# Kernel optimization log

Hardware: AMD Instinct MI355X
Metric: run time of the kernel (lower is better)

The kernel has to match this reference:

```python
import jax, jax.numpy as jnp
import numpy as np

N, D_IN, D_OUT = 8192, 1024, 1024

def setup_inputs() -> dict:
    key = jax.random.key(0)
    k1, k2, k3, k4 = jax.random.split(key, 4)
    scale = 1.0 / np.sqrt(D_IN).astype(np.float32)
    return {
        "X": jax.random.normal(k1, (N, D_IN), dtype=jnp.float32),
        "W_Q": jax.random.normal(k2, (D_IN, D_OUT), dtype=jnp.float32) * scale,
        "W_K": jax.random.normal(k3, (D_IN, D_OUT), dtype=jnp.float32) * scale,
        "W_V": jax.random.normal(k4, (D_IN, D_OUT), dtype=jnp.float32) * scale,
    }

def reference(X, W_Q, W_K, W_V):
    # Manual single-head self-attention over the N rows of X.
    Q = X @ W_Q            # [N, d_out]
    Kmat = X @ W_K         # [N, d_out]
    V = X @ W_V            # [N, d_out]
    inv_sqrt_d = jnp.asarray(1.0 / np.sqrt(W_Q.shape[1]), dtype=Q.dtype)
    scores = (Q @ Kmat.T) * inv_sqrt_d            # [N, N]
    attn = jax.nn.softmax(scores, axis=-1)        # row-wise softmax (Keras default axis=-1)
    return attn @ V                               # [N, d_out]
```

## Files before the change

kernel.cpp:

```cpp
#include <hip/hip_runtime.h>

#define N_ROWS 8192
#define D_DIM  1024
#define SM_SHIFT 4.0f

typedef _Float16 f16;
typedef _Float16 f16x8 __attribute__((ext_vector_type(8)));
typedef _Float16 f16x4 __attribute__((ext_vector_type(4)));
typedef float    f32x4 __attribute__((ext_vector_type(4)));

__device__ __forceinline__ void gload16(const void* g, void* l) {
  __builtin_amdgcn_global_load_lds(
      (const __attribute__((address_space(1))) void*)g,
      (__attribute__((address_space(3))) void*)l, 16, 0, 0);
}

__device__ __forceinline__ int xcd_swz(int bid, int nb) {
  return (bid & 7) * (nb >> 3) + (bid >> 3);
}

__device__ __forceinline__ void tile2d4(int bid, int ny_t, int& nx, int& ny) {
  const int v = xcd_swz(bid, 32 * ny_t);
  const int g = v >> 4, w = v & 15;
  const int gpc = ny_t >> 2;
  const int gx = g / gpc, gy = g - gx * gpc;
  nx = gx * 4 + (w & 3);
  ny = gy * 4 + (w >> 2);
}

__global__ __launch_bounds__(256) void f32_to_f16_kernel(
    const float* __restrict__ in, f16* __restrict__ out, int n4) {
  for (int i = blockIdx.x * blockDim.x + threadIdx.x; i < n4;
       i += gridDim.x * blockDim.x) {
    float4 x = ((const float4*)in)[i];
    f16x4 h = {(f16)x.x, (f16)x.y, (f16)x.z, (f16)x.w};
    ((f16x4*)out)[i] = h;
  }
}

__global__ __launch_bounds__(256) void transpose_w_kernel(
    const float* __restrict__ w0, const float* __restrict__ w1,
    const float* __restrict__ w2, f16* __restrict__ WT) {
  const float* W = (blockIdx.z == 0) ? w0 : (blockIdx.z == 1) ? w1 : w2;
  f16* T = WT + (size_t)blockIdx.z * D_DIM * D_DIM;
  __shared__ float tile[64][65];
  const int r0 = blockIdx.y * 64, c0 = blockIdx.x * 64;
  const int t = threadIdx.x;
#pragma unroll
  for (int rep = 0; rep < 16; ++rep) {
    int idx = rep * 256 + t;
    int r = idx >> 6, c = idx & 63;
    tile[r][c] = W[(size_t)(r0 + r) * D_DIM + (c0 + c)];
  }
  __syncthreads();
#pragma unroll
  for (int rep = 0; rep < 16; ++rep) {
    int idx = rep * 256 + t;
    int r = idx >> 6, c = idx & 63;
    T[(size_t)(c0 + r) * D_DIM + (r0 + c)] = (f16)tile[c][r];
  }
}

template <bool SWAP>
__device__ __forceinline__ void mainloop256(const f16* __restrict__ Ag, int lda,
                                            const f16* __restrict__ Bg,
                                            int ldbt, int nk, f16* LA, f16* LB,
                                            f32x4 (&acc)[8][4], int tid) {
  const int lane = tid & 63;
  const int wr = tid >> 8, wc = (tid >> 6) & 3;
  const int ro = lane & 15;
  const int jj0 = (((lane >> 4) ^ (ro & 7)) << 4);
  const int rs = tid >> 3;
  const int ce = ((tid & 7) ^ (rs & 7)) * 8;
  const f16* a[4];
  const f16* b[4];
#pragma unroll
  for (int s = 0; s < 4; ++s) {
    a[s] = Ag + (size_t)(rs + 64 * s) * lda + ce;
    b[s] = Bg + (size_t)(rs + 64 * s) * ldbt + ce;
  }
  char* la = (char*)LA;
  char* lb = (char*)LB;
  const int t16 = tid * 16;

  auto stage = [&](int buf) {
    char* A = la + buf * 32768;
    char* B = lb + buf * 32768;
#pragma unroll
    for (int s = 0; s < 4; ++s) {
      gload16(a[s], A + s * 8192 + t16);
      gload16(b[s], B + s * 8192 + t16);
    }
#pragma unroll
    for (int s = 0; s < 4; ++s) {
      a[s] += 64;
      b[s] += 64;
    }
  };

  f16x8 af[4], bf[4];
  auto readA = [&](const char* ab, int h, int jo) {
#pragma unroll
    for (int j = 0; j < 4; ++j)
      af[j] = *(const f16x8*)(ab + (wr * 128 + h * 64 + j * 16 + ro) * 128 + jo);
  };
  auto readB = [&](const char* bb, int jo) {
#pragma unroll
    for (int ni = 0; ni < 4; ++ni)
      bf[ni] = *(const f16x8*)(bb + (wc * 64 + ni * 16 + ro) * 128 + jo);
  };

#define PHASE_TAIL(H)                                                     \
  __builtin_amdgcn_s_barrier();                                           \
  __builtin_amdgcn_sched_barrier(0);                                      \
  asm volatile("s_waitcnt lgkmcnt(0)" ::: "memory");                      \
  __builtin_amdgcn_sched_barrier(0);                                      \
  __builtin_amdgcn_s_setprio(1);                                          \
  _Pragma("unroll") for (int j = 0; j < 4; ++j)                           \
  _Pragma("unroll") for (int ni = 0; ni < 4; ++ni)                        \
      acc[(H) * 4 + j][ni] =                                              \
          SWAP ? __builtin_amdgcn_mfma_f32_16x16x32_f16(bf[ni], af[j],    \
                                                        acc[(H) * 4 + j][ni], \
                                                        0, 0, 0)          \
               : __builtin_amdgcn_mfma_f32_16x16x32_f16(af[j], bf[ni],    \
                                                        acc[(H) * 4 + j][ni], \
                                                        0, 0, 0);         \
  __builtin_amdgcn_s_setprio(0);

  stage(0);
  if (nk > 1) {
    stage(1);
    asm volatile("s_waitcnt vmcnt(8)" ::: "memory");
  } else {
    asm volatile("s_waitcnt vmcnt(0)" ::: "memory");
  }
  __builtin_amdgcn_s_barrier();
  __builtin_amdgcn_sched_barrier(0);

  for (int kt = 0; kt < nk; ++kt) {
    const int buf = kt & 1;
    const char* ab = la + buf * 32768;
    const char* bb = lb + buf * 32768;
    readA(ab, 0, jj0);
    readB(bb, jj0);
    PHASE_TAIL(0)
    readA(ab, 1, jj0);
    PHASE_TAIL(1)
    readA(ab, 0, jj0 ^ 64);
    readB(bb, jj0 ^ 64);
    PHASE_TAIL(0)
    readA(ab, 1, jj0 ^ 64);
    PHASE_TAIL(1)
    __builtin_amdgcn_s_barrier();
    __builtin_amdgcn_sched_barrier(0);
    if (kt + 2 < nk) stage(buf);
    if (kt + 1 < nk) {
      if (kt + 2 < nk)
        asm volatile("s_waitcnt vmcnt(8)" ::: "memory");
      else
        asm volatile("s_waitcnt vmcnt(0)" ::: "memory");
      __builtin_amdgcn_s_barrier();
      __builtin_amdgcn_sched_barrier(0);
    }
  }
#undef PHASE_TAIL
}

#define ACC_INIT8(acc)                                \
  _Pragma("unroll") for (int i = 0; i < 8; ++i)       \
      _Pragma("unroll") for (int j = 0; j < 4; ++j)   \
          acc[i][j] = (f32x4){0.f, 0.f, 0.f, 0.f};

__global__ __launch_bounds__(512, 2) void gemm_qkv(
    const f16* __restrict__ Xh, const f16* __restrict__ WT,
    f16* __restrict__ Q, f16* __restrict__ Kh, f16* __restrict__ VT) {
  __shared__ f16 LA[2][16384], LB[2][16384];
  const int v = xcd_swz(blockIdx.x, 384);
  const int z = v >> 7, r = v & 127;
  const int nx = r & 3, ny = r >> 2;
  const int tid = threadIdx.x, lane = tid & 63;
  const int wr = tid >> 8, wc = (tid >> 6) & 3;
  const int ro = lane & 15, rq = (lane >> 4) * 4;

  const f16* A = Xh + (size_t)ny * 256 * D_DIM;
  const f16* B = WT + (size_t)z * D_DIM * D_DIM + (size_t)nx * 256 * D_DIM;

  f32x4 acc[8][4];
  ACC_INIT8(acc);
  if (z < 2) {
    mainloop256<true>(A, D_DIM, B, D_DIM, D_DIM / 64, &LA[0][0], &LB[0][0],
                      acc, tid);
    f16* C = z ? Kh : Q;
#pragma unroll
    for (int mi = 0; mi < 8; ++mi) {
      const size_t xr = ny * 256 + wr * 128 + mi * 16 + ro;
#pragma unroll
      for (int ni = 0; ni < 4; ++ni) {
        f16x4 pk;
#pragma unroll
        for (int rr = 0; rr < 4; ++rr) pk[rr] = (f16)acc[mi][ni][rr];
        *(f16x4*)&C[xr * D_DIM + nx * 256 + wc * 64 + ni * 16 + rq] = pk;
      }
    }
  } else {
    mainloop256<false>(A, D_DIM, B, D_DIM, D_DIM / 64, &LA[0][0], &LB[0][0],
                       acc, tid);
#pragma unroll
    for (int mi = 0; mi < 8; ++mi)
#pragma unroll
      for (int ni = 0; ni < 4; ++ni) {
        f16x4 pk;
#pragma unroll
        for (int rr = 0; rr < 4; ++rr) pk[rr] = (f16)acc[mi][ni][rr];
        const size_t d = nx * 256 + wc * 64 + ni * 16 + ro;
        *(f16x4*)&VT[d * N_ROWS + ny * 256 + wr * 128 + mi * 16 + rq] = pk;
      }
  }
}

__global__ __launch_bounds__(512, 2) void gemm_s_exp(
    const f16* __restrict__ Q, const f16* __restrict__ Kh, f16* __restrict__ S,
    float* __restrict__ Lpart, int nyb) {
  __shared__ f16 LA[2][16384], LB[2][16384];
  int nx, ny;
  tile2d4(blockIdx.x, nyb, nx, ny);
  const int tid = threadIdx.x, lane = tid & 63;
  const int wr = tid >> 8, wc = (tid >> 6) & 3;
  const int ro = lane & 15, rq = (lane >> 4) * 4;

  f32x4 acc[8][4];
  ACC_INIT8(acc);
  mainloop256<true>(Q + (size_t)ny * 256 * D_DIM, D_DIM,
                    Kh + (size_t)nx * 256 * D_DIM, D_DIM, D_DIM / 64,
                    &LA[0][0], &LB[0][0], acc, tid);

  const float sc = 0.03125f;
#pragma unroll
  for (int mi = 0; mi < 8; ++mi) {
    const size_t q = ny * 256 + wr * 128 + mi * 16 + ro;
    f16* srow = S + q * N_ROWS + nx * 256 + wc * 64 + rq;
    float rs = 0.f;
#pragma unroll
    for (int ni = 0; ni < 4; ++ni) {
      f16x4 pk;
#pragma unroll
      for (int rr = 0; rr < 4; ++rr) {
        const float p = __expf(acc[mi][ni][rr] * sc - SM_SHIFT);
        rs += p;
        pk[rr] = (f16)p;
      }
      *(f16x4*)&srow[ni * 16] = pk;
    }
    rs += __shfl_xor(rs, 16, 64);
    rs += __shfl_xor(rs, 32, 64);
    if (lane < 16) Lpart[q * 128 + nx * 4 + wc] = rs;
  }
}

__global__ __launch_bounds__(256) void reduce_l(const float* __restrict__ Lpart,
                                                float* __restrict__ linv,
                                                int rows) {
  const int w = (blockIdx.x * 256 + threadIdx.x) >> 6;
  const int lane = threadIdx.x & 63;
  if (w >= rows) return;
  const float* p = Lpart + (size_t)w * 128;
  float s = p[lane] + p[lane + 64];
#pragma unroll
  for (int o = 32; o > 0; o >>= 1) s += __shfl_xor(s, o, 64);
  if (lane == 0) linv[w] = 1.0f / s;
}

__global__ __launch_bounds__(512, 2) void gemm_pv(const f16* __restrict__ S,
                                                  const f16* __restrict__ VT,
                                                  float* __restrict__ Ppart,
                                                  int nyb, int KS, int chunk) {
  __shared__ f16 LA[2][16384], LB[2][16384];
  const int nid = xcd_swz(blockIdx.x, (int)gridDim.x);
  const int nx = nid & 3, ny = (nid >> 2) % nyb, z = (nid >> 2) / nyb;
  const int tid = threadIdx.x, lane = tid & 63;
  const int wr = tid >> 8, wc = (tid >> 6) & 3;
  const int ro = lane & 15, rq = (lane >> 4) * 4;

  f32x4 acc[8][4];
  ACC_INIT8(acc);
  mainloop256<true>(S + (size_t)ny * 256 * N_ROWS + (size_t)z * KS, N_ROWS,
                    VT + (size_t)nx * 256 * N_ROWS + (size_t)z * KS, N_ROWS,
                    KS / 64, &LA[0][0], &LB[0][0], acc, tid);

  float* out = Ppart + (size_t)z * chunk * D_DIM;
#pragma unroll
  for (int mi = 0; mi < 8; ++mi) {
    const size_t q = ny * 256 + wr * 128 + mi * 16 + ro;
#pragma unroll
    for (int ni = 0; ni < 4; ++ni)
      *(f32x4*)&out[q * D_DIM + nx * 256 + wc * 64 + ni * 16 + rq] =
          acc[mi][ni];
  }
}

__global__ __launch_bounds__(256) void reduce_o(
    const float* __restrict__ Ppart, const float* __restrict__ linv,
    float* __restrict__ O, int rows, int sk) {
  const int n4 = rows * 256;
  const int stride = gridDim.x * blockDim.x;
  for (int i = blockIdx.x * 256 + threadIdx.x; i < n4; i += stride) {
    f32x4 s = ((const f32x4*)Ppart)[i];
    for (int t = 1; t < sk; ++t) s += ((const f32x4*)Ppart)[(size_t)t * n4 + i];
    const float il = linv[i >> 8];
    ((f32x4*)O)[i] = s * il;
  }
}

extern "C" void kernel_launch(void* const* d_in, const int* in_sizes, int n_in,
                              void* d_out, int out_size, void* d_ws,
                              size_t ws_size, hipStream_t stream) {
  (void)in_sizes;
  (void)n_in;
  (void)out_size;
  const float* X = (const float*)d_in[0];
  const float* WQ = (const float*)d_in[1];
  const float* WK = (const float*)d_in[2];
  const float* WV = (const float*)d_in[3];
  float* O = (float*)d_out;

  const size_t fixedA = (size_t)N_ROWS * D_DIM * 2 + 3ull * D_DIM * D_DIM * 2;
  int chunk = 1024, sk = 1;
  const int pref[][2] = {{8192, 2}, {4096, 2}, {2048, 2}, {8192, 1},
                         {4096, 1}, {2048, 1}, {1024, 1}};
  for (int i = 0; i < 7; ++i) {
    const int c = pref[i][0], s = pref[i][1];
    size_t R = (size_t)s * c * D_DIM * 4;
    if (R < fixedA) R = fixedA;
    const size_t need = R + 3ull * N_ROWS * D_DIM * 2 + (size_t)c * N_ROWS * 2 +
                        (size_t)c * 128 * 4 + (size_t)c * 4 + 4096;
    if (need <= ws_size) {
      chunk = c;
      sk = s;
      break;
    }
  }

  char* base = (char*)d_ws;
  f16* Xh = (f16*)base;
  f16* WT = (f16*)(base + (size_t)N_ROWS * D_DIM * 2);
  float* Ppart = (float*)base;
  size_t R = (size_t)sk * chunk * D_DIM * 4;
  if (R < fixedA) R = fixedA;
  char* p = base + ((R + 255) & ~(size_t)255);
  f16* Q = (f16*)p;
  p += (size_t)N_ROWS * D_DIM * 2;
  f16* Kh = (f16*)p;
  p += (size_t)N_ROWS * D_DIM * 2;
  f16* VT = (f16*)p;
  p += (size_t)N_ROWS * D_DIM * 2;
  f16* S = (f16*)p;
  p += (size_t)chunk * N_ROWS * 2;
  float* Lpart = (float*)p;
  p += (size_t)chunk * 128 * 4;
  float* linv = (float*)p;

  f32_to_f16_kernel<<<2048, 256, 0, stream>>>(X, Xh, N_ROWS * D_DIM / 4);
  transpose_w_kernel<<<dim3(16, 16, 3), 256, 0, stream>>>(WQ, WK, WV, WT);
  gemm_qkv<<<384, 512, 0, stream>>>(Xh, WT, Q, Kh, VT);

  const int KS = N_ROWS / sk;
  for (int mc = 0; mc < N_ROWS; mc += chunk) {
    const int nyb = chunk / 256;
    gemm_s_exp<<<32 * nyb, 512, 0, stream>>>(Q + (size_t)mc * D_DIM, Kh, S,
                                             Lpart, nyb);
    reduce_l<<<(chunk + 3) / 4, 256, 0, stream>>>(Lpart, linv, chunk);
    gemm_pv<<<4 * nyb * sk, 512, 0, stream>>>(S, VT, Ppart, nyb, KS, chunk);
    reduce_o<<<1024, 256, 0, stream>>>(Ppart, linv, O + (size_t)mc * D_DIM,
                                       chunk, sk);
  }
}
```

Measured before the change: 410.2 us.

## Split tile staging into halves interleaved with MFMA phases in GEMM loop

Each K-tile stage is split into two halves of global-to-LDS loads. The halves are issued between the MFMA phases of the current tile, instead of in one burst after compute. Prefetch depth drops from two tiles ahead to one, with fine-grained vmcnt waits ordered so each LDS half is resident before it is read. An extra barrier at the end of every phase protects the double buffer. The aim is to spread memory traffic across compute, at the cost of more barriers and less latency slack.

```diff
diff --git a/kernel.cpp b/kernel.cpp
--- a/kernel.cpp
+++ b/kernel.cpp
@@ -83,14 +83,21 @@
   char* lb = (char*)LB;
   const int t16 = tid * 16;
 
-  auto stage = [&](int buf) {
+  auto stage_p0 = [&](int buf) {
     char* A = la + buf * 32768;
     char* B = lb + buf * 32768;
-#pragma unroll
-    for (int s = 0; s < 4; ++s) {
-      gload16(a[s], A + s * 8192 + t16);
-      gload16(b[s], B + s * 8192 + t16);
-    }
+    gload16(a[0], A + t16);
+    gload16(a[2], A + 16384 + t16);
+    gload16(b[0], B + t16);
+    gload16(b[1], B + 8192 + t16);
+  };
+  auto stage_p1 = [&](int buf) {
+    char* A = la + buf * 32768;
+    char* B = lb + buf * 32768;
+    gload16(b[2], B + 16384 + t16);
+    gload16(b[3], B + 24576 + t16);
+    gload16(a[1], A + 8192 + t16);
+    gload16(a[3], A + 24576 + t16);
 #pragma unroll
     for (int s = 0; s < 4; ++s) {
       a[s] += 64;
@@ -111,7 +118,7 @@
   };
 
 #define PHASE_TAIL(H)                                                     \
-  __builtin_amdgcn_s_barrier();                                           \
+  __builtin_amdgcn_s_barrier();                             \
   __builtin_amdgcn_sched_barrier(0);                                      \
   asm volatile("s_waitcnt lgkmcnt(0)" ::: "memory");                      \
   __builtin_amdgcn_sched_barrier(0);                                      \
@@ -125,15 +132,13 @@
                : __builtin_amdgcn_mfma_f32_16x16x32_f16(af[j], bf[ni],    \
                                                         acc[(H) * 4 + j][ni], \
                                                         0, 0, 0);         \
-  __builtin_amdgcn_s_setprio(0);
-
-  stage(0);
-  if (nk > 1) {
-    stage(1);
-    asm volatile("s_waitcnt vmcnt(8)" ::: "memory");
-  } else {
-    asm volatile("s_waitcnt vmcnt(0)" ::: "memory");
-  }
+  __builtin_amdgcn_s_setprio(0);                                          \
+  __builtin_amdgcn_s_barrier();                             \
+  __builtin_amdgcn_sched_barrier(0);
+
+  stage_p0(0);
+  stage_p1(0);
+  asm volatile("s_waitcnt vmcnt(0)" ::: "memory");
   __builtin_amdgcn_s_barrier();
   __builtin_amdgcn_sched_barrier(0);
 
@@ -141,27 +146,25 @@
     const int buf = kt & 1;
     const char* ab = la + buf * 32768;
     const char* bb = lb + buf * 32768;
+    const bool more = (kt + 1 < nk);
     readA(ab, 0, jj0);
     readB(bb, jj0);
+    if (more) {
+      stage_p0(buf ^ 1);
+      asm volatile("s_waitcnt vmcnt(4)" ::: "memory");
+    } else {
+      asm volatile("s_waitcnt vmcnt(0)" ::: "memory");
+    }
     PHASE_TAIL(0)
     readA(ab, 1, jj0);
+    if (more) stage_p1(buf ^ 1);
     PHASE_TAIL(1)
     readA(ab, 0, jj0 ^ 64);
     readB(bb, jj0 ^ 64);
     PHASE_TAIL(0)
     readA(ab, 1, jj0 ^ 64);
+    asm volatile("s_waitcnt vmcnt(2)" ::: "memory");
     PHASE_TAIL(1)
-    __builtin_amdgcn_s_barrier();
-    __builtin_amdgcn_sched_barrier(0);
-    if (kt + 2 < nk) stage(buf);
-    if (kt + 1 < nk) {
-      if (kt + 2 < nk)
-        asm volatile("s_waitcnt vmcnt(8)" ::: "memory");
-      else
-        asm volatile("s_waitcnt vmcnt(0)" ::: "memory");
-      __builtin_amdgcn_s_barrier();
-      __builtin_amdgcn_sched_barrier(0);
-    }
   }
 #undef PHASE_TAIL
 }
```

Result: faster. 391.6 us (-4.5%).
